# Optimization experiments

Hardware: AMD Instinct MI355X
Metric: run time of the kernel (lower is better)

## Reference

```python
import jax, jax.numpy as jnp
import numpy as np

B, N, F = 2, 2048, 1024
H = 16
DH = F // H  # features per head = 64
SCALE = 1.0 / np.sqrt(DH)


def setup_inputs() -> dict:
    key = jax.random.key(0)
    ks = jax.random.split(key, 11)
    s = 0.02
    return {
        "q": jax.random.normal(ks[0], (B, N, F), dtype=jnp.float32),
        "k": jax.random.normal(ks[1], (B, N, F), dtype=jnp.float32),
        "v": jax.random.normal(ks[2], (B, N, F), dtype=jnp.float32),
        "Wq": jax.random.normal(ks[3], (F, F), dtype=jnp.float32) * s,
        "bq": jnp.zeros((F,), dtype=jnp.float32),
        "Wk": jax.random.normal(ks[4], (F, F), dtype=jnp.float32) * s,
        "bk": jnp.zeros((F,), dtype=jnp.float32),
        "Wv": jax.random.normal(ks[5], (F, F), dtype=jnp.float32) * s,
        "bv": jnp.zeros((F,), dtype=jnp.float32),
        "Wo": jax.random.normal(ks[6], (F, F), dtype=jnp.float32) * s,
        "bo": jnp.zeros((F,), dtype=jnp.float32),
    }


def reference(q, k, v, Wq, bq, Wk, bk, Wv, bv, Wo, bo):
    b = q.shape[0]
    # projections, split into heads: [B, H, N, DH]
    qh = (q @ Wq + bq).reshape(b, -1, H, DH).transpose(0, 2, 1, 3)
    kh = (k @ Wk + bk).reshape(b, -1, H, DH).transpose(0, 2, 1, 3)
    vh = (v @ Wv + bv).reshape(b, -1, H, DH).transpose(0, 2, 1, 3)
    # scaled dot-product attention
    attn = jnp.einsum("bhqd,bhkd->bhqk", qh * SCALE, kh)
    attn = jax.nn.softmax(attn, axis=-1)
    out = jnp.einsum("bhqk,bhkd->bhqd", attn, vh)
    # merge heads: [B, Nq, F]
    out = out.transpose(0, 2, 1, 3).reshape(b, -1, H * DH)
    return out @ Wo + bo
```

## Files before the change

### kernel.cpp

```cpp
#include <hip/hip_runtime.h>
#include <hip/hip_bf16.h>

typedef float f32x4  __attribute__((ext_vector_type(4)));
typedef float f32x16 __attribute__((ext_vector_type(16)));
typedef short s16x8  __attribute__((ext_vector_type(8)));
typedef unsigned int u32;
typedef unsigned short u16;
typedef u16 u16x4 __attribute__((ext_vector_type(4)));
typedef u32 u32x4 __attribute__((ext_vector_type(4)));

#define DEVI static __device__ __forceinline__

constexpr int BB   = 2;
constexpr int SEQ  = 2048;
constexpr int FD   = 1024;
constexpr int NH   = 16;
constexpr int DHD  = 64;
constexpr int MROWS = BB * SEQ;

DEVI u16 f2bf(float x){
  __hip_bfloat16 h = __float2bfloat16(x);
  return __builtin_bit_cast(u16, h);
}
DEVI float bf2f(u16 u){
  return __bfloat162float(__builtin_bit_cast(__hip_bfloat16, u));
}
DEVI u32 cvtpk(float lo, float hi){
  u32 r;
  asm("v_cvt_pk_bf16_f32 %0, %1, %2" : "=v"(r) : "v"(lo), "v"(hi));
  return r;
}
DEVI float max3f(float a, float b, float c){
  float r;
  asm("v_max3_f32 %0, %1, %2, %3" : "=v"(r) : "v"(a), "v"(b), "v"(c));
  return r;
}

DEVI void mfma_bf16(f32x4& acc, s16x8 a, s16x8 b){
  asm("v_mfma_f32_16x16x32_bf16 %0, %1, %2, %0" : "+v"(acc) : "v"(a), "v"(b));
}
DEVI void mfma32(f32x16& acc, s16x8 a, s16x8 b){
  asm("v_mfma_f32_32x32x16_bf16 %0, %1, %2, %0" : "+v"(acc) : "v"(a), "v"(b));
}
DEVI void plswap(u32& a, u32& b){
  asm("v_permlane32_swap_b32 %0, %1" : "+v"(a), "+v"(b));
}

#define AS1C(p) ((const __attribute__((address_space(1))) void*)(p))
#define AS3(p)  ((__attribute__((address_space(3))) void*)(p))

#define VMCNT(n)  asm volatile("s_waitcnt vmcnt(" #n ")" ::: "memory")
#define LGKMCNT0  asm volatile("s_waitcnt lgkmcnt(0)" ::: "memory")
DEVI void barrier(){ __builtin_amdgcn_s_barrier(); __builtin_amdgcn_sched_barrier(0); }

__global__ __launch_bounds__(256) void prep_all(
    const float* __restrict__ q, const float* __restrict__ k,
    const float* __restrict__ v, u16* __restrict__ abf,
    const float* __restrict__ W0, const float* __restrict__ W1,
    const float* __restrict__ W2, const float* __restrict__ W3,
    u16* __restrict__ T0, u16* __restrict__ T1,
    u16* __restrict__ T2, u16* __restrict__ T3)
{
  __shared__ float tile[64][65];
  const int bid = blockIdx.x;

  if (bid < 6144){
    const size_t n1 = (size_t)MROWS * FD;
    const size_t i  = ((size_t)bid * 256 + threadIdx.x) * 8;
    const float* src = (i < n1) ? q + i : (i < 2*n1 ? k + (i - n1) : v + (i - 2*n1));
    float4 v0 = *reinterpret_cast<const float4*>(src);
    float4 v1 = *reinterpret_cast<const float4*>(src + 4);
    s16x8 r;
    r[0]=(short)f2bf(v0.x); r[1]=(short)f2bf(v0.y);
    r[2]=(short)f2bf(v0.z); r[3]=(short)f2bf(v0.w);
    r[4]=(short)f2bf(v1.x); r[5]=(short)f2bf(v1.y);
    r[6]=(short)f2bf(v1.z); r[7]=(short)f2bf(v1.w);
    *reinterpret_cast<s16x8*>(abf + i) = r;
    return;
  }

  const int wb = bid - 6144;
  const int z  = wb >> 8;
  const float* W = z==0?W0 : z==1?W1 : z==2?W2 : W3;
  u16* Th       = z==0?T0 : z==1?T1 : z==2?T2 : T3;

  const int kb = ((wb >> 4) & 15) * 64, nb = (wb & 15) * 64;
  const int t  = threadIdx.x;
  const int r  = t >> 2, c0 = (t & 3) * 16;

  const float* src = W + (size_t)(kb + r) * FD + nb + c0;
  #pragma unroll
  for (int i = 0; i < 16; i += 4){
    float4 vv = *reinterpret_cast<const float4*>(src + i);
    tile[r][c0+i+0] = vv.x; tile[r][c0+i+1] = vv.y;
    tile[r][c0+i+2] = vv.z; tile[r][c0+i+3] = vv.w;
  }
  __syncthreads();

  s16x8 hA, hB;
  #pragma unroll
  for (int i = 0; i < 8; i++){
    hA[i] = (short)f2bf(tile[c0 + i][r]);
    hB[i] = (short)f2bf(tile[c0 + 8 + i][r]);
  }
  const size_t o = (size_t)(nb + r) * FD + kb + c0;
  *reinterpret_cast<s16x8*>(Th + o)     = hA;
  *reinterpret_cast<s16x8*>(Th + o + 8) = hB;
}

DEVI s16x8 ldsT(const u16* base, int row, int g){
  const char* p = reinterpret_cast<const char*>(base);
  return *reinterpret_cast<const s16x8*>(p + (row << 6) + ((g ^ ((row >> 1) & 3)) << 4));
}

__global__ __launch_bounds__(256, 3) void qkv_gemm(
    const u16* __restrict__ Abase,
    const u16* __restrict__ Wq, const u16* __restrict__ Wk, const u16* __restrict__ Wv,
    const float* __restrict__ bq, const float* __restrict__ bk, const float* __restrict__ bv,
    u16* __restrict__ Q2, u16* __restrict__ K2, u16* __restrict__ Vt2)
{
  __shared__ u16 sA[2][128*32];
  __shared__ u16 sW[2][128*32];

  const int bid  = blockIdx.x;
  const int xcd  = bid & 7, idx = bid >> 3;
  const int strip = xcd * 12 + (idx >> 3);
  const int nb   = idx & 7;
  const int z    = strip >> 5, my = strip & 31;

  const u16* Ap     = Abase + (size_t)z * MROWS * FD;
  const u16*  Wh    = z==0?Wq : z==1?Wk : Wv;
  const float* bias = z==0?bq : z==1?bk : bv;
  u16* outp         = z==0?Q2 : z==1?K2 : Vt2;
  const float oscale = (z==0) ? 0.125f : 1.0f;
  const bool  tr     = (z==2);

  const int t    = threadIdx.x;
  const int nb0  = nb * 128, mb0 = my * 128;
  const int lane = t & 63, w = t >> 6;
  const int r16  = lane & 15, g = lane >> 4;
  const int wm   = (w >> 1) * 64, wn = (w & 1) * 64;

  const int sRow   = lane >> 2;
  const int sChunk = (lane & 3);

  auto stage = [&](int buf, int kb){
    #pragma unroll
    for (int i = 0; i < 2; i++){
      const int row = w*32 + i*16 + sRow;
      const int gch = sChunk ^ ((row >> 1) & 3);
      const u16* ag = Ap + (size_t)(mb0 + row) * FD + kb + gch*8;
      const u16* wg = Wh + (size_t)(nb0 + row) * FD + kb + gch*8;
      __builtin_amdgcn_global_load_lds(AS1C(ag), AS3(&sA[buf][(w*32 + i*16)*32]), 16, 0, 0);
      __builtin_amdgcn_global_load_lds(AS1C(wg), AS3(&sW[buf][(w*32 + i*16)*32]), 16, 0, 0);
    }
  };

  f32x4 acc[4][4] = {};

  stage(0, 0);
  stage(1, 32);
  VMCNT(4);
  barrier();

  for (int it = 0; it < FD/32; it++){
    const int buf = it & 1;

    s16x8 a[4], bh[4];
    #pragma unroll
    for (int i = 0; i < 4; i++)
      a[i]  = ldsT(sA[buf], wm + i*16 + r16, g);
    #pragma unroll
    for (int j = 0; j < 4; j++)
      bh[j] = ldsT(sW[buf], wn + j*16 + r16, g);
    LGKMCNT0;
    barrier();

    if (it + 2 < FD/32) stage(buf, (it + 2) * 32);

    __builtin_amdgcn_s_setprio(1);
    #pragma unroll
    for (int i = 0; i < 4; i++)
      #pragma unroll
      for (int j = 0; j < 4; j++)
        mfma_bf16(acc[i][j], a[i], bh[j]);
    __builtin_amdgcn_s_setprio(0);

    if (it + 2 < FD/32) { VMCNT(4); }
    else                { VMCNT(0); }
    barrier();
  }

  #pragma unroll
  for (int i = 0; i < 4; i++){
    #pragma unroll
    for (int j = 0; j < 4; j++){
      const int ccol = nb0 + wn + j*16 + r16;
      const float bv = bias[ccol];
      #pragma unroll
      for (int r = 0; r < 4; r++){
        const int m = mb0 + wm + i*16 + g*4 + r;
        const float v = (acc[i][j][r] + bv) * oscale;
        const int b = m >> 11, n = m & (SEQ - 1);
        const int h = ccol >> 6, d = ccol & 63;
        const size_t o = tr ? ((size_t)(b*NH + h)*DHD + d)*SEQ + n
                            : ((size_t)(b*NH + h)*SEQ + n)*DHD + d;
        outp[o] = f2bf(v);
      }
    }
  }
}

__global__ __launch_bounds__(256, 3) void ogemm_k(
    const u16* __restrict__ Ap, const u16* __restrict__ Wh,
    const float* __restrict__ bias, float* __restrict__ outp)
{
  __shared__ u16 sA[2][64*32];
  __shared__ u16 sW[2][128*32];

  const int bid  = blockIdx.x;
  const int xcd  = bid & 7, idx = bid >> 3;
  const int my   = xcd * 8 + (idx >> 3);
  const int nb   = idx & 7;

  const int t    = threadIdx.x;
  const int nb0  = nb * 128, mb0 = my * 64;
  const int lane = t & 63, w = t >> 6;
  const int r16  = lane & 15, g = lane >> 4;
  const int wm   = (w >> 1) * 32, wn = (w & 1) * 64;

  const int sRow   = lane >> 2;
  const int sChunk = (lane & 3);

  auto stage = [&](int buf, int kb){
    {
      const int row = w*16 + sRow;
      const int gch = sChunk ^ ((row >> 1) & 3);
      const u16* ag = Ap + (size_t)(mb0 + row) * FD + kb + gch*8;
      __builtin_amdgcn_global_load_lds(AS1C(ag), AS3(&sA[buf][(w*16)*32]), 16, 0, 0);
    }
    #pragma unroll
    for (int i = 0; i < 2; i++){
      const int row = w*32 + i*16 + sRow;
      const int gch = sChunk ^ ((row >> 1) & 3);
      const u16* wg = Wh + (size_t)(nb0 + row) * FD + kb + gch*8;
      __builtin_amdgcn_global_load_lds(AS1C(wg), AS3(&sW[buf][(w*32 + i*16)*32]), 16, 0, 0);
    }
  };

  f32x4 acc[2][4] = {};

  stage(0, 0);
  stage(1, 32);
  VMCNT(3);
  barrier();

  for (int it = 0; it < FD/32; it++){
    const int buf = it & 1;

    s16x8 a[2], bh[4];
    #pragma unroll
    for (int i = 0; i < 2; i++)
      a[i]  = ldsT(sA[buf], wm + i*16 + r16, g);
    #pragma unroll
    for (int j = 0; j < 4; j++)
      bh[j] = ldsT(sW[buf], wn + j*16 + r16, g);
    LGKMCNT0;
    barrier();

    if (it + 2 < FD/32) stage(buf, (it + 2) * 32);

    __builtin_amdgcn_s_setprio(1);
    #pragma unroll
    for (int i = 0; i < 2; i++)
      #pragma unroll
      for (int j = 0; j < 4; j++)
        mfma_bf16(acc[i][j], a[i], bh[j]);
    __builtin_amdgcn_s_setprio(0);

    if (it + 2 < FD/32) { VMCNT(3); }
    else                { VMCNT(0); }
    barrier();
  }

  #pragma unroll
  for (int i = 0; i < 2; i++){
    #pragma unroll
    for (int j = 0; j < 4; j++){
      const int ccol = nb0 + wn + j*16 + r16;
      const float bv = bias[ccol];
      #pragma unroll
      for (int r = 0; r < 4; r++){
        const int m = mb0 + wm + i*16 + g*4 + r;
        outp[(size_t)m * FD + ccol] = acc[i][j][r] + bv;
      }
    }
  }
}

__global__ __launch_bounds__(512, 4) void attn_k(
    const u16* __restrict__ Q2, const u16* __restrict__ K2, const u16* __restrict__ Vt2,
    u16* __restrict__ AOh)
{
  __shared__ u16 smem[2][2][2][64*64];

  const int bid = blockIdx.x + 16 * blockIdx.y;
  const int qt  = bid >> 5;
  const int bh  = (bid & 7) * 4 + ((bid >> 3) & 3);

  const int t = threadIdx.x, w = t >> 6, lane = t & 63;
  const int grp = w >> 2, gw = w & 3;
  const int l31 = lane & 31, hi = lane >> 5;

  const u16* Kb = K2  + (size_t)bh * SEQ * DHD;
  const u16* Vb = Vt2 + (size_t)bh * DHD * SEQ;

  const int srow8  = lane >> 3;
  const int schunk = ((lane & 7) ^ srow8) * 8;

  const int qrow = qt*128 + gw*32 + l31;
  const u16* Qrow = Q2 + ((size_t)bh * SEQ + qrow) * DHD;
  s16x8 qf[4];
  #pragma unroll
  for (int dk = 0; dk < 4; dk++)
    qf[dk] = *reinterpret_cast<const s16x8*>(Qrow + dk*16 + hi*8);

  f32x16 ot0 = {}, ot1 = {};
  float mrun = -1e30f, lrun = 0.f;

  auto stage_tile = [&](int buf, int kt){
    #pragma unroll
    for (int i = 0; i < 2; i++){
      const int row = gw*16 + i*8 + srow8;
      const u16* kg = Kb + (size_t)(kt*64 + row) * DHD + schunk;
      const u16* vg = Vb + (size_t)row * SEQ + kt*64 + schunk;
      __builtin_amdgcn_global_load_lds(AS1C(kg), AS3(&smem[0][grp][buf][(gw*16 + i*8)*64]), 16, 0, 0);
      __builtin_amdgcn_global_load_lds(AS1C(vg), AS3(&smem[1][grp][buf][(gw*16 + i*8)*64]), 16, 0, 0);
    }
  };
  auto lds16 = [](const u16* base, int row, int colbyte) -> s16x8 {
    int off = (row << 7) + colbyte;
    off ^= (row & 7) << 4;
    return *reinterpret_cast<const s16x8*>(reinterpret_cast<const char*>(base) + off);
  };

  constexpr int NIT = SEQ / 64 / 2;
  stage_tile(0, grp);
  __syncthreads();

  for (int i = 0; i < NIT; i++){
    const int buf = i & 1;
    if (i + 1 < NIT) stage_tile(buf ^ 1, 2*(i+1) + grp);
    const u16* sK = &smem[0][grp][buf][0];
    const u16* sV = &smem[1][grp][buf][0];

    f32x16 st0 = {}, st1 = {};
    __builtin_amdgcn_s_setprio(1);
    #pragma unroll
    for (int dk = 0; dk < 4; dk++){
      s16x8 kf0 = lds16(sK, l31,      dk*32 + hi*16);
      s16x8 kf1 = lds16(sK, 32 + l31, dk*32 + hi*16);
      mfma32(st0, kf0, qf[dk]);
      mfma32(st1, kf1, qf[dk]);
    }
    __builtin_amdgcn_s_setprio(0);

    float a0 = max3f(st0[0],  st0[1],  st0[2]);
    float a1 = max3f(st0[3],  st0[4],  st0[5]);
    float a2 = max3f(st0[6],  st0[7],  st0[8]);
    float a3 = max3f(st0[9],  st0[10], st0[11]);
    float a4 = max3f(st0[12], st0[13], st0[14]);
    float a5 = max3f(st1[0],  st1[1],  st1[2]);
    float a6 = max3f(st1[3],  st1[4],  st1[5]);
    float a7 = max3f(st1[6],  st1[7],  st1[8]);
    float a8 = max3f(st1[9],  st1[10], st1[11]);
    float a9 = max3f(st1[12], st1[13], st1[14]);
    float b0 = max3f(a0, a1, a2);
    float b1 = max3f(a3, a4, a5);
    float b2 = max3f(a6, a7, a8);
    float b3 = max3f(a9, st0[15], st1[15]);
    float pmax = fmaxf(max3f(b0, b1, b2), b3);
    pmax = fmaxf(pmax, __shfl_xor(pmax, 32, 64));

    if (!__all(pmax <= mrun + 8.f)){
      float mnew = fmaxf(mrun, pmax);
      float alp = __expf(mrun - mnew);
      mrun = mnew;
      lrun *= alp;
      #pragma unroll
      for (int r = 0; r < 16; r++){ ot0[r] *= alp; ot1[r] *= alp; }
    }

    #pragma unroll
    for (int r = 0; r < 16; r++){
      st0[r] = __expf(st0[r] - mrun);
      st1[r] = __expf(st1[r] - mrun);
    }
    float s8[8];
    #pragma unroll
    for (int r = 0; r < 8; r++)
      s8[r] = (st0[r] + st0[r+8]) + (st1[r] + st1[r+8]);
    float psum = ((s8[0]+s8[1])+(s8[2]+s8[3])) + ((s8[4]+s8[5])+(s8[6]+s8[7]));
    psum += __shfl_xor(psum, 32, 64);
    lrun += psum;

    u32 pw[16];
    #pragma unroll
    for (int g2 = 0; g2 < 4; g2++){
      pw[g2*2+0]   = cvtpk(st0[g2*4+0], st0[g2*4+1]);
      pw[g2*2+1]   = cvtpk(st0[g2*4+2], st0[g2*4+3]);
      pw[8+g2*2+0] = cvtpk(st1[g2*4+0], st1[g2*4+1]);
      pw[8+g2*2+1] = cvtpk(st1[g2*4+2], st1[g2*4+3]);
    }
    s16x8 pb[4];
    #pragma unroll
    for (int ks = 0; ks < 4; ks++){
      const int e = (ks>>1)*8 + (ks&1)*4;
      u32 w0 = pw[e+0], w1 = pw[e+1], w2 = pw[e+2], w3 = pw[e+3];
      plswap(w0, w2);
      plswap(w1, w3);
      u32x4 wv = { w0, w1, w2, w3 };
      pb[ks] = __builtin_bit_cast(s16x8, wv);
    }

    __builtin_amdgcn_s_setprio(1);
    #pragma unroll
    for (int ks = 0; ks < 4; ks++){
      s16x8 vf0 = lds16(sV, l31,      ks*32 + hi*16);
      s16x8 vf1 = lds16(sV, 32 + l31, ks*32 + hi*16);
      mfma32(ot0, vf0, pb[ks]);
      mfma32(ot1, vf1, pb[ks]);
    }
    __builtin_amdgcn_s_setprio(0);

    __syncthreads();
  }

  float* sO = reinterpret_cast<float*>(&smem[0][0][0][0]);
  float* sM = reinterpret_cast<float*>(&smem[0][0][0][0]) + 128*68;
  const int ql = gw*32 + l31;

  if (grp == 1){
    #pragma unroll
    for (int r4 = 0; r4 < 4; r4++){
      const int d0 = r4*8 + hi*4;
      #pragma unroll
      for (int j = 0; j < 4; j++){
        sO[ql*68 + d0 + j]      = ot0[r4*4+j];
        sO[ql*68 + 32 + d0 + j] = ot1[r4*4+j];
      }
    }
    if (hi == 0){ sM[ql*2+0] = mrun; sM[ql*2+1] = lrun; }
  }
  __syncthreads();
  if (grp == 0){
    const float m1 = sM[ql*2+0], l1 = sM[ql*2+1];
    const float M  = fmaxf(mrun, m1);
    const float w0 = __expf(mrun - M), w1e = __expf(m1 - M);
    const float inv = 1.0f / (lrun*w0 + l1*w1e);

    const int b = bh >> 4, h = bh & 15;
    u16* orow = AOh + ((size_t)b*SEQ + qrow) * FD + h*64;
    #pragma unroll
    for (int r4 = 0; r4 < 4; r4++){
      const int d0 = r4*8 + hi*4;
      u16x4 v0, v1;
      #pragma unroll
      for (int j = 0; j < 4; j++){
        v0[j] = f2bf((ot0[r4*4+j]*w0 + sO[ql*68 + d0 + j]*w1e) * inv);
        v1[j] = f2bf((ot1[r4*4+j]*w0 + sO[ql*68 + 32 + d0 + j]*w1e) * inv);
      }
      *reinterpret_cast<u16x4*>(orow + d0)      = v0;
      *reinterpret_cast<u16x4*>(orow + 32 + d0) = v1;
    }
  }
}

extern "C" void kernel_launch(void* const* d_in, const int* in_sizes, int n_in,
                              void* d_out, int out_size, void* d_ws, size_t ws_size,
                              hipStream_t stream)
{
  const float* q  = (const float*)d_in[0];
  const float* k  = (const float*)d_in[1];
  const float* v  = (const float*)d_in[2];
  const float* Wq = (const float*)d_in[3];
  const float* bq = (const float*)d_in[4];
  const float* Wk = (const float*)d_in[5];
  const float* bk = (const float*)d_in[6];
  const float* Wv = (const float*)d_in[7];
  const float* bv = (const float*)d_in[8];
  const float* Wo = (const float*)d_in[9];
  const float* bo = (const float*)d_in[10];
  float* out = (float*)d_out;
  (void)in_sizes; (void)n_in; (void)out_size; (void)ws_size;

  char* ws = (char*)d_ws;
  size_t off = 0;
  auto alloc = [&](size_t bytes) -> char* {
    char* p = ws + off;
    off += (bytes + 255) & ~(size_t)255;
    return p;
  };
  const size_t WB = (size_t)FD * FD * sizeof(u16);
  u16* WqTh = (u16*)alloc(WB);
  u16* WkTh = (u16*)alloc(WB);
  u16* WvTh = (u16*)alloc(WB);
  u16* WoTh = (u16*)alloc(WB);
  const size_t QB = (size_t)BB * NH * SEQ * DHD * sizeof(u16);
  u16* Q2  = (u16*)alloc(QB);
  u16* K2  = (u16*)alloc(QB);
  u16* Vt2 = (u16*)alloc(QB);
  const size_t AB = (size_t)BB * SEQ * FD * sizeof(u16);
  u16* AOh = (u16*)alloc(AB);
  u16* Abf = (u16*)alloc(3 * AB);

  prep_all<<<dim3(7168), 256, 0, stream>>>(q, k, v, Abf,
                                           Wq, Wk, Wv, Wo,
                                           WqTh, WkTh, WvTh, WoTh);

  qkv_gemm<<<dim3(768), 256, 0, stream>>>(Abf, WqTh, WkTh, WvTh,
                                          bq, bk, bv, Q2, K2, Vt2);

  attn_k<<<dim3(16,32), 512, 0, stream>>>(Q2, K2, Vt2, AOh);

  ogemm_k<<<dim3(512), 256, 0, stream>>>(AOh, WoTh, bo, out);
}
```

Measured before the change: 139.0 us.

## Fuse fp32-to-bf16 activation conversion into QKV GEMM operand loading

Removes the separate pass that converted the q/k/v activations to bf16 in a workspace. The QKV GEMM now streams fp32 activations straight into LDS with swizzled direct loads and converts them to packed bf16 when reading fragments, and the prep kernel only handles weights. This drops a full read-write round trip of the activations, in exchange for twice the LDS footprint and global bytes per A tile inside the GEMM, plus conversion ALU work in the inner loop.

```diff
diff --git a/kernel.cpp b/kernel.cpp
--- a/kernel.cpp
+++ b/kernel.cpp
@@ -53,47 +53,27 @@
 #define LGKMCNT0  asm volatile("s_waitcnt lgkmcnt(0)" ::: "memory")
 DEVI void barrier(){ __builtin_amdgcn_s_barrier(); __builtin_amdgcn_sched_barrier(0); }
 
-__global__ __launch_bounds__(256) void prep_all(
-    const float* __restrict__ q, const float* __restrict__ k,
-    const float* __restrict__ v, u16* __restrict__ abf,
+__global__ __launch_bounds__(256) void wprep_all(
     const float* __restrict__ W0, const float* __restrict__ W1,
     const float* __restrict__ W2, const float* __restrict__ W3,
     u16* __restrict__ T0, u16* __restrict__ T1,
     u16* __restrict__ T2, u16* __restrict__ T3)
 {
-  __shared__ float tile[64][65];
-  const int bid = blockIdx.x;
-
-  if (bid < 6144){
-    const size_t n1 = (size_t)MROWS * FD;
-    const size_t i  = ((size_t)bid * 256 + threadIdx.x) * 8;
-    const float* src = (i < n1) ? q + i : (i < 2*n1 ? k + (i - n1) : v + (i - 2*n1));
-    float4 v0 = *reinterpret_cast<const float4*>(src);
-    float4 v1 = *reinterpret_cast<const float4*>(src + 4);
-    s16x8 r;
-    r[0]=(short)f2bf(v0.x); r[1]=(short)f2bf(v0.y);
-    r[2]=(short)f2bf(v0.z); r[3]=(short)f2bf(v0.w);
-    r[4]=(short)f2bf(v1.x); r[5]=(short)f2bf(v1.y);
-    r[6]=(short)f2bf(v1.z); r[7]=(short)f2bf(v1.w);
-    *reinterpret_cast<s16x8*>(abf + i) = r;
-    return;
-  }
-
-  const int wb = bid - 6144;
-  const int z  = wb >> 8;
+  const int z = blockIdx.z;
   const float* W = z==0?W0 : z==1?W1 : z==2?W2 : W3;
   u16* Th       = z==0?T0 : z==1?T1 : z==2?T2 : T3;
 
-  const int kb = ((wb >> 4) & 15) * 64, nb = (wb & 15) * 64;
+  __shared__ float tile[64][65];
+  const int kb = blockIdx.x * 64, nb = blockIdx.y * 64;
   const int t  = threadIdx.x;
   const int r  = t >> 2, c0 = (t & 3) * 16;
 
   const float* src = W + (size_t)(kb + r) * FD + nb + c0;
   #pragma unroll
   for (int i = 0; i < 16; i += 4){
-    float4 vv = *reinterpret_cast<const float4*>(src + i);
-    tile[r][c0+i+0] = vv.x; tile[r][c0+i+1] = vv.y;
-    tile[r][c0+i+2] = vv.z; tile[r][c0+i+3] = vv.w;
+    float4 v = *reinterpret_cast<const float4*>(src + i);
+    tile[r][c0+i+0] = v.x; tile[r][c0+i+1] = v.y;
+    tile[r][c0+i+2] = v.z; tile[r][c0+i+3] = v.w;
   }
   __syncthreads();
 
@@ -114,13 +94,13 @@
 }
 
 __global__ __launch_bounds__(256, 3) void qkv_gemm(
-    const u16* __restrict__ Abase,
+    const float* __restrict__ qp, const float* __restrict__ kp, const float* __restrict__ vp,
     const u16* __restrict__ Wq, const u16* __restrict__ Wk, const u16* __restrict__ Wv,
     const float* __restrict__ bq, const float* __restrict__ bk, const float* __restrict__ bv,
     u16* __restrict__ Q2, u16* __restrict__ K2, u16* __restrict__ Vt2)
 {
-  __shared__ u16 sA[2][128*32];
-  __shared__ u16 sW[2][128*32];
+  __shared__ float sAf[2][128*32];
+  __shared__ u16   sW [2][128*32];
 
   const int bid  = blockIdx.x;
   const int xcd  = bid & 7, idx = bid >> 3;
@@ -128,7 +108,7 @@
   const int nb   = idx & 7;
   const int z    = strip >> 5, my = strip & 31;
 
-  const u16* Ap     = Abase + (size_t)z * MROWS * FD;
+  const float* Ap   = z==0?qp : z==1?kp : vp;
   const u16*  Wh    = z==0?Wq : z==1?Wk : Wv;
   const float* bias = z==0?bq : z==1?bk : bv;
   u16* outp         = z==0?Q2 : z==1?K2 : Vt2;
@@ -141,26 +121,44 @@
   const int r16  = lane & 15, g = lane >> 4;
   const int wm   = (w >> 1) * 64, wn = (w & 1) * 64;
 
+  const int aRow   = lane >> 3;
+  const int aChunk = ((lane & 7) ^ aRow) * 4;
   const int sRow   = lane >> 2;
   const int sChunk = (lane & 3);
 
   auto stage = [&](int buf, int kb){
+    #pragma unroll
+    for (int i = 0; i < 4; i++){
+      const int row = w*32 + i*8 + aRow;
+      const float* ag = Ap + (size_t)(mb0 + row) * FD + kb + aChunk;
+      __builtin_amdgcn_global_load_lds(AS1C(ag), AS3(&sAf[buf][(w*32 + i*8)*32]), 16, 0, 0);
+    }
     #pragma unroll
     for (int i = 0; i < 2; i++){
       const int row = w*32 + i*16 + sRow;
       const int gch = sChunk ^ ((row >> 1) & 3);
-      const u16* ag = Ap + (size_t)(mb0 + row) * FD + kb + gch*8;
       const u16* wg = Wh + (size_t)(nb0 + row) * FD + kb + gch*8;
-      __builtin_amdgcn_global_load_lds(AS1C(ag), AS3(&sA[buf][(w*32 + i*16)*32]), 16, 0, 0);
       __builtin_amdgcn_global_load_lds(AS1C(wg), AS3(&sW[buf][(w*32 + i*16)*32]), 16, 0, 0);
     }
+  };
+  auto ldsA = [&](const float* base, int row, int gg) -> s16x8 {
+    const char* p = reinterpret_cast<const char*>(base);
+    const int roff = row << 7, sw = (row & 7) << 4;
+    f32x4 lo = *reinterpret_cast<const f32x4*>(p + roff + ((gg*32)      ^ sw));
+    f32x4 hi = *reinterpret_cast<const f32x4*>(p + roff + ((gg*32 + 16) ^ sw));
+    u32 w0 = cvtpk(lo[0], lo[1]);
+    u32 w1 = cvtpk(lo[2], lo[3]);
+    u32 w2 = cvtpk(hi[0], hi[1]);
+    u32 w3 = cvtpk(hi[2], hi[3]);
+    u32x4 wv = { w0, w1, w2, w3 };
+    return __builtin_bit_cast(s16x8, wv);
   };
 
   f32x4 acc[4][4] = {};
 
   stage(0, 0);
   stage(1, 32);
-  VMCNT(4);
+  VMCNT(6);
   barrier();
 
   for (int it = 0; it < FD/32; it++){
@@ -169,7 +167,7 @@
     s16x8 a[4], bh[4];
     #pragma unroll
     for (int i = 0; i < 4; i++)
-      a[i]  = ldsT(sA[buf], wm + i*16 + r16, g);
+      a[i]  = ldsA(sAf[buf], wm + i*16 + r16, g);
     #pragma unroll
     for (int j = 0; j < 4; j++)
       bh[j] = ldsT(sW[buf], wn + j*16 + r16, g);
@@ -186,7 +184,7 @@
         mfma_bf16(acc[i][j], a[i], bh[j]);
     __builtin_amdgcn_s_setprio(0);
 
-    if (it + 2 < FD/32) { VMCNT(4); }
+    if (it + 2 < FD/32) { VMCNT(6); }
     else                { VMCNT(0); }
     barrier();
   }
@@ -512,13 +510,11 @@
   u16* Vt2 = (u16*)alloc(QB);
   const size_t AB = (size_t)BB * SEQ * FD * sizeof(u16);
   u16* AOh = (u16*)alloc(AB);
-  u16* Abf = (u16*)alloc(3 * AB);
-
-  prep_all<<<dim3(7168), 256, 0, stream>>>(q, k, v, Abf,
-                                           Wq, Wk, Wv, Wo,
-                                           WqTh, WkTh, WvTh, WoTh);
-
-  qkv_gemm<<<dim3(768), 256, 0, stream>>>(Abf, WqTh, WkTh, WvTh,
+
+  wprep_all<<<dim3(16,16,4), 256, 0, stream>>>(Wq, Wk, Wv, Wo,
+                                               WqTh, WkTh, WvTh, WoTh);
+
+  qkv_gemm<<<dim3(768), 256, 0, stream>>>(q, k, v, WqTh, WkTh, WvTh,
                                           bq, bk, bv, Q2, K2, Vt2);
 
   attn_k<<<dim3(16,32), 512, 0, stream>>>(Q2, K2, Vt2, AOh);
```

New measurement: 136.4 us. About the same (-1.8%).
